# Optimization experiments

Hardware: AMD Instinct MI355X
Metric: run time of the kernel (lower is better)

The kernel has to match this reference:

```python
import jax, jax.numpy as jnp
import numpy as np

B, V = 128, 128000

def setup_inputs() -> dict:
    key = jax.random.key(0)
    k1, k2, k3, k4 = jax.random.split(key, 4)
    logits = jax.random.normal(k1, (B, V), dtype=jnp.float32) * 4.0
    k = jax.random.randint(k2, (B,), 1, 64).astype(jnp.int32)
    p = jax.random.uniform(k3, (B,), dtype=jnp.float32, minval=0.5, maxval=1.0)
    # torch's q.exponential_(): Exp(1) noise = -log(U)
    u = jax.random.uniform(k4, (B, V), dtype=jnp.float32, minval=1e-10, maxval=1.0)
    exp_noise = -jnp.log(u)
    return {"logits": logits, "k": k, "p": p, "exp_noise": exp_noise}

def _apply_top_k_top_p(logits, k, p):
    # ascending sort, matching torch logits.sort(descending=False)
    idx = jnp.argsort(logits, axis=-1)                       # [B, V]
    logits_sort = jnp.take_along_axis(logits, idx, axis=-1)  # [B, V]
    # top-k: threshold is the (V-k)-th smallest value; everything below -> -inf
    thr_pos = (logits.shape[-1] - k.astype(jnp.int32))[:, None]       # [B, 1]
    thr = jnp.take_along_axis(logits_sort, thr_pos, axis=-1)          # [B, 1]
    logits_sort = jnp.where(logits_sort < thr, -jnp.inf, logits_sort)
    # top-p: drop the low-probability tail whose cumulative mass <= 1 - p
    probs_sort = jax.nn.softmax(logits_sort, axis=-1)
    probs_sum = jnp.cumsum(probs_sort, axis=-1)
    top_p_mask = probs_sum <= (1.0 - p)[:, None]
    top_p_mask = top_p_mask.at[:, -1].set(False)  # always keep the max token
    logits_sort = jnp.where(top_p_mask, -jnp.inf, logits_sort)
    # scatter filtered values back to original token positions
    inv = jnp.argsort(idx, axis=-1)
    return jnp.take_along_axis(logits_sort, inv, axis=-1)

def reference(logits, k, p, exp_noise):
    filtered = _apply_top_k_top_p(logits, k, p)
    probs = jax.nn.softmax(filtered.astype(jnp.float32), axis=-1)
    # random_sample: argmax(probs / Exp(1)) == Gumbel-trick categorical sample
    return jnp.argmax(probs / exp_noise, axis=-1)
```

## Files before the change

kernel.cpp:

```cpp
#include <hip/hip_runtime.h>
#include <stdint.h>

#define B_ROWS 128
#define V_COLS 128000
#define BPR 16
#define SLICE (V_COLS / BPR)
#define N4 (SLICE / 4)
#define NTHR 256
#define CAP 2048

__device__ __forceinline__ uint32_t f2u_bits(uint32_t x) {
    return (x & 0x80000000u) ? ~x : (x | 0x80000000u);
}
__device__ __forceinline__ float u2f(uint32_t u) {
    uint32_t x = (u & 0x80000000u) ? (u & 0x7FFFFFFFu) : ~u;
    return __uint_as_float(x);
}

__device__ __forceinline__ bool pair_gt(uint32_t au, uint32_t ai, uint32_t bu, uint32_t bi) {
    return (au > bu) || (au == bu && ai > bi);
}

__device__ __forceinline__ void merge64(uint32_t& au, uint32_t& ai,
                                        uint32_t bu, uint32_t bi, int lane) {
    uint32_t ou = (uint32_t)__shfl_xor((int)bu, 63, 64);
    uint32_t oi = (uint32_t)__shfl_xor((int)bi, 63, 64);
    if (!pair_gt(au, ai, ou, oi)) { au = ou; ai = oi; }
    #pragma unroll
    for (int j = 32; j >= 1; j >>= 1) {
        uint32_t cu = (uint32_t)__shfl_xor((int)au, j, 64);
        uint32_t ci = (uint32_t)__shfl_xor((int)ai, j, 64);
        bool sg = pair_gt(au, ai, cu, ci);
        bool keep = ((lane & j) == 0) ? sg : !sg;
        if (!keep) { au = cu; ai = ci; }
    }
}

__device__ __forceinline__ void wave_sort64(uint32_t& u, uint32_t& i, int lane) {
    #pragma unroll
    for (int ksz = 2; ksz <= 64; ksz <<= 1) {
        #pragma unroll
        for (int j = ksz >> 1; j > 0; j >>= 1) {
            uint32_t ou = (uint32_t)__shfl_xor((int)u, j, 64);
            uint32_t oi = (uint32_t)__shfl_xor((int)i, j, 64);
            bool asc   = (lane & ksz) == 0;
            bool lower = (lane & j) == 0;
            bool sg = pair_gt(u, i, ou, oi);
            bool keep = (asc == lower) ? sg : !sg;
            if (!keep) { u = ou; i = oi; }
        }
    }
}

__device__ __forceinline__ void lds_bitonic_desc(uint32_t* su, uint32_t* si, int NP) {
    const int tid = threadIdx.x;
    for (int ksz = 2; ksz <= NP; ksz <<= 1) {
        for (int j = ksz >> 1; j > 0; j >>= 1) {
            __syncthreads();
            for (int i = tid; i < NP; i += NTHR) {
                int ixj = i ^ j;
                if (ixj > i) {
                    uint32_t ua = su[i], ub = su[ixj];
                    uint32_t ia = si[i], ib = si[ixj];
                    bool a_lt = (ua < ub) || (ua == ub && ia < ib);
                    if (((i & ksz) == 0) ? a_lt : !a_lt) {
                        su[i] = ub; su[ixj] = ua;
                        si[i] = ib; si[ixj] = ia;
                    }
                }
            }
        }
    }
    __syncthreads();
}

__global__ __launch_bounds__(NTHR) void topk_slice_kernel(
    const float* __restrict__ logits, uint2* __restrict__ out_run)
{
    __shared__ uint32_t s_u[CAP];
    __shared__ uint32_t s_i[CAP];
    __shared__ uint32_t s_T[4];
    __shared__ int s_cnt;

    const int blk = blockIdx.x;
    const int row = blk >> 4;
    const int q   = blk & 15;
    const int tid = threadIdx.x;
    const int lane = tid & 63;
    const int wv   = tid >> 6;

    if (tid == 0) s_cnt = 0;

    const uint4* src = (const uint4*)(logits + (size_t)row * V_COLS + (size_t)q * SLICE);

    uint4 g[8];
    #pragma unroll
    for (int j = 0; j < 8; ++j) {
        int i4 = j * NTHR + tid;
        i4 = (i4 < N4) ? i4 : (N4 - 1);
        g[j] = src[i4];
    }
    #pragma unroll
    for (int j = 0; j < 8; ++j) {
        g[j].x = f2u_bits(g[j].x); g[j].y = f2u_bits(g[j].y);
        g[j].z = f2u_bits(g[j].z); g[j].w = f2u_bits(g[j].w);
    }
    if (7 * NTHR + tid >= N4) { g[7].x = 0u; g[7].y = 0u; g[7].z = 0u; g[7].w = 0u; }

    uint32_t mx = 0u;
    #pragma unroll
    for (int j = 0; j < 8; ++j) {
        uint32_t a = g[j].x > g[j].y ? g[j].x : g[j].y;
        uint32_t b = g[j].z > g[j].w ? g[j].z : g[j].w;
        a = a > b ? a : b;
        mx = mx > a ? mx : a;
    }

    uint32_t v = mx;
    #pragma unroll
    for (int ksz = 2; ksz <= 64; ksz <<= 1) {
        #pragma unroll
        for (int j = ksz >> 1; j > 0; j >>= 1) {
            uint32_t o = (uint32_t)__shfl_xor((int)v, j, 64);
            bool asc   = (lane & ksz) == 0;
            bool lower = (lane & j) == 0;
            uint32_t mn = (v < o) ? v : o;
            uint32_t mh = (v < o) ? o : v;
            v = (asc == lower) ? mn : mh;
        }
    }
    uint32_t Tw = (uint32_t)__shfl((int)v, 48, 64);
    if (lane == 0) s_T[wv] = Tw;
    __syncthreads();
    uint32_t T0 = s_T[0] < s_T[1] ? s_T[0] : s_T[1];
    uint32_t T1 = s_T[2] < s_T[3] ? s_T[2] : s_T[3];
    uint32_t T = T0 < T1 ? T0 : T1;

    #pragma unroll
    for (int j = 0; j < 8; ++j) {
        const int base = q * SLICE + (j * NTHR + tid) * 4;
        uint32_t uu0 = g[j].x, uu1 = g[j].y, uu2 = g[j].z, uu3 = g[j].w;
        if (uu0 >= T && uu0 != 0u) { int p = atomicAdd(&s_cnt, 1); if (p < CAP) { s_u[p] = uu0; s_i[p] = (uint32_t)(base + 0); } }
        if (uu1 >= T && uu1 != 0u) { int p = atomicAdd(&s_cnt, 1); if (p < CAP) { s_u[p] = uu1; s_i[p] = (uint32_t)(base + 1); } }
        if (uu2 >= T && uu2 != 0u) { int p = atomicAdd(&s_cnt, 1); if (p < CAP) { s_u[p] = uu2; s_i[p] = (uint32_t)(base + 2); } }
        if (uu3 >= T && uu3 != 0u) { int p = atomicAdd(&s_cnt, 1); if (p < CAP) { s_u[p] = uu3; s_i[p] = (uint32_t)(base + 3); } }
    }
    __syncthreads();
    int cnt = s_cnt; if (cnt > CAP) cnt = CAP;

    if (cnt <= 256) {
        for (int i = cnt + tid; i < 256; i += NTHR) { s_u[i] = 0u; s_i[i] = 0xFFFFFFFFu; }
        __syncthreads();
        uint32_t cu = s_u[wv * 64 + lane];
        uint32_t ci = s_i[wv * 64 + lane];
        wave_sort64(cu, ci, lane);
        s_u[wv * 64 + lane] = cu;
        s_i[wv * 64 + lane] = ci;
        __syncthreads();
        if (wv == 0) {
            uint32_t b1u = s_u[64 + lane];  uint32_t b1i = s_i[64 + lane];
            uint32_t b2u = s_u[128 + lane]; uint32_t b2i = s_i[128 + lane];
            uint32_t b3u = s_u[192 + lane]; uint32_t b3i = s_i[192 + lane];
            merge64(cu, ci, b1u, b1i, lane);
            merge64(b2u, b2i, b3u, b3i, lane);
            merge64(cu, ci, b2u, b2i, lane);
            out_run[blk * 64 + lane] = make_uint2(cu, ci);
        }
    } else {
        int NP = 256; while (NP < cnt) NP <<= 1;
        for (int i = cnt + tid; i < NP; i += NTHR) { s_u[i] = 0u; s_i[i] = 0xFFFFFFFFu; }
        lds_bitonic_desc(s_u, s_i, NP);
        if (tid < 64) out_run[blk * 64 + tid] = make_uint2(s_u[tid], s_i[tid]);
    }
}

__global__ __launch_bounds__(NTHR) void sample_kernel(
    const uint2* __restrict__ runs,
    const int* __restrict__ kk, const float* __restrict__ pp,
    const float* __restrict__ noise, int* __restrict__ out)
{
    __shared__ uint32_t m_u[4 * 64];
    __shared__ uint32_t m_i[4 * 64];
    const int row = blockIdx.x;
    const int tid = threadIdx.x;
    const int lane = tid & 63;
    const int wv   = tid >> 6;

    const uint2* br = runs + (size_t)row * (BPR * 64);

    uint2 r0 = br[(wv * 4 + 0) * 64 + lane];
    uint2 r1 = br[(wv * 4 + 1) * 64 + lane];
    uint2 r2 = br[(wv * 4 + 2) * 64 + lane];
    uint2 r3 = br[(wv * 4 + 3) * 64 + lane];
    uint32_t a0u = r0.x, a0i = r0.y;
    uint32_t a1u = r1.x, a1i = r1.y;
    uint32_t a2u = r2.x, a2i = r2.y;
    uint32_t a3u = r3.x, a3i = r3.y;
    merge64(a0u, a0i, a1u, a1i, lane);
    merge64(a2u, a2i, a3u, a3i, lane);
    merge64(a0u, a0i, a2u, a2i, lane);
    m_u[wv * 64 + lane] = a0u;
    m_i[wv * 64 + lane] = a0i;
    __syncthreads();

    if (wv == 0) {
        uint32_t b1u = m_u[64 + lane];  uint32_t b1i = m_i[64 + lane];
        uint32_t b2u = m_u[128 + lane]; uint32_t b2i = m_i[128 + lane];
        uint32_t b3u = m_u[192 + lane]; uint32_t b3i = m_i[192 + lane];
        merge64(a0u, a0i, b1u, b1i, lane);
        merge64(b2u, b2i, b3u, b3i, lane);
        merge64(a0u, a0i, b2u, b2i, lane);

        float v2 = u2f(a0u);
        uint32_t tok = a0i;
        int k = kk[row];
        if (k > 64) k = 64;
        float p = pp[row];

        float thrv = __shfl(v2, k - 1, 64);
        bool kept = v2 >= thrv;
        float m = __shfl(v2, 0, 64);
        float e = kept ? expf(v2 - m) : 0.0f;

        float denom = e;
        #pragma unroll
        for (int off = 1; off < 64; off <<= 1) denom += __shfl_xor(denom, off, 64);
        float prob = e / denom;

        float cums = prob;
        #pragma unroll
        for (int off = 1; off < 64; off <<= 1) {
            float o = __shfl_down(cums, off, 64);
            cums += (lane + off < 64) ? o : 0.0f;
        }
        bool masked = (cums <= 1.0f - p) && (lane != 0);
        bool surv = kept && !masked;

        float e2 = surv ? e : 0.0f;
        float denom2 = e2;
        #pragma unroll
        for (int off = 1; off < 64; off <<= 1) denom2 += __shfl_xor(denom2, off, 64);

        float score = -1.0f;
        uint32_t bidx = 0xFFFFFFFFu;
        if (surv) {
            float nz = noise[(size_t)row * V_COLS + tok];
            score = (e / denom2) / nz;
            bidx = tok;
        }
        #pragma unroll
        for (int off = 1; off < 64; off <<= 1) {
            float os = __shfl_xor(score, off, 64);
            uint32_t oi = __shfl_xor(bidx, off, 64);
            if (os > score || (os == score && oi < bidx)) { score = os; bidx = oi; }
        }
        if (lane == 0) out[row] = (int)bidx;
    }
}

extern "C" void kernel_launch(void* const* d_in, const int* in_sizes, int n_in,
                              void* d_out, int out_size, void* d_ws, size_t ws_size,
                              hipStream_t stream) {
    const float* logits = (const float*)d_in[0];
    const int* kk       = (const int*)d_in[1];
    const float* pp     = (const float*)d_in[2];
    const float* noise  = (const float*)d_in[3];
    int* out            = (int*)d_out;

    uint2* ws_run = (uint2*)d_ws;

    topk_slice_kernel<<<B_ROWS * BPR, NTHR, 0, stream>>>(logits, ws_run);
    sample_kernel<<<B_ROWS, NTHR, 0, stream>>>(ws_run, kk, pp, noise, out);
}
```

Measured before the change: 27.95 us.

## Halve blocks per row and compute exact block-wide top-64 threshold

Splits each row across 8 blocks instead of 16, so every thread loads 16 uint4 vectors instead of 8. The candidate threshold is now the exact 64th-largest of all per-thread maxima in the block, found with a bitonic merge of the four sorted wave lists, rather than the minimum of four per-wave 16th-largest values. This is meant to shrink the candidate set and the sort work, and it halves the runs the sample kernel has to merge. The cost is fewer blocks (1024 instead of 2048), higher register pressure from the 16 loaded vectors, and two extra barriers.

```diff
diff --git a/kernel.cpp b/kernel.cpp
--- a/kernel.cpp
+++ b/kernel.cpp
@@ -3,10 +3,11 @@
 
 #define B_ROWS 128
 #define V_COLS 128000
-#define BPR 16
+#define BPR 8
 #define SLICE (V_COLS / BPR)
 #define N4 (SLICE / 4)
 #define NTHR 256
+#define LPT 16
 #define CAP 2048
 
 __device__ __forceinline__ uint32_t f2u_bits(uint32_t x) {
@@ -33,6 +34,18 @@
         bool sg = pair_gt(au, ai, cu, ci);
         bool keep = ((lane & j) == 0) ? sg : !sg;
         if (!keep) { au = cu; ai = ci; }
+    }
+}
+
+__device__ __forceinline__ void merge64v(uint32_t& au, uint32_t bu, int lane) {
+    uint32_t ou = (uint32_t)__shfl_xor((int)bu, 63, 64);
+    au = au > ou ? au : ou;
+    #pragma unroll
+    for (int j = 32; j >= 1; j >>= 1) {
+        uint32_t cu = (uint32_t)__shfl_xor((int)au, j, 64);
+        uint32_t mx = au > cu ? au : cu;
+        uint32_t mn = au > cu ? cu : au;
+        au = ((lane & j) == 0) ? mx : mn;
     }
 }
 
@@ -79,12 +92,12 @@
 {
     __shared__ uint32_t s_u[CAP];
     __shared__ uint32_t s_i[CAP];
-    __shared__ uint32_t s_T[4];
+    __shared__ uint32_t s_Tval;
     __shared__ int s_cnt;
 
     const int blk = blockIdx.x;
-    const int row = blk >> 4;
-    const int q   = blk & 15;
+    const int row = blk >> 3;
+    const int q   = blk & 7;
     const int tid = threadIdx.x;
     const int lane = tid & 63;
     const int wv   = tid >> 6;
@@ -93,23 +106,25 @@
 
     const uint4* src = (const uint4*)(logits + (size_t)row * V_COLS + (size_t)q * SLICE);
 
-    uint4 g[8];
-    #pragma unroll
-    for (int j = 0; j < 8; ++j) {
+    uint4 g[LPT];
+    #pragma unroll
+    for (int j = 0; j < LPT; ++j) {
         int i4 = j * NTHR + tid;
         i4 = (i4 < N4) ? i4 : (N4 - 1);
         g[j] = src[i4];
     }
     #pragma unroll
-    for (int j = 0; j < 8; ++j) {
+    for (int j = 0; j < LPT; ++j) {
         g[j].x = f2u_bits(g[j].x); g[j].y = f2u_bits(g[j].y);
         g[j].z = f2u_bits(g[j].z); g[j].w = f2u_bits(g[j].w);
     }
-    if (7 * NTHR + tid >= N4) { g[7].x = 0u; g[7].y = 0u; g[7].z = 0u; g[7].w = 0u; }
+    if ((LPT - 1) * NTHR + tid >= N4) {
+        g[LPT - 1].x = 0u; g[LPT - 1].y = 0u; g[LPT - 1].z = 0u; g[LPT - 1].w = 0u;
+    }
 
     uint32_t mx = 0u;
     #pragma unroll
-    for (int j = 0; j < 8; ++j) {
+    for (int j = 0; j < LPT; ++j) {
         uint32_t a = g[j].x > g[j].y ? g[j].x : g[j].y;
         uint32_t b = g[j].z > g[j].w ? g[j].z : g[j].w;
         a = a > b ? a : b;
@@ -129,15 +144,23 @@
             v = (asc == lower) ? mn : mh;
         }
     }
-    uint32_t Tw = (uint32_t)__shfl((int)v, 48, 64);
-    if (lane == 0) s_T[wv] = Tw;
-    __syncthreads();
-    uint32_t T0 = s_T[0] < s_T[1] ? s_T[0] : s_T[1];
-    uint32_t T1 = s_T[2] < s_T[3] ? s_T[2] : s_T[3];
-    uint32_t T = T0 < T1 ? T0 : T1;
-
-    #pragma unroll
-    for (int j = 0; j < 8; ++j) {
+    s_u[wv * 64 + (63 - lane)] = v;
+    __syncthreads();
+
+    if (wv == 0) {
+        uint32_t t0 = s_u[lane];
+        merge64v(t0, s_u[64 + lane], lane);
+        uint32_t t2 = s_u[128 + lane];
+        merge64v(t2, s_u[192 + lane], lane);
+        merge64v(t0, t2, lane);
+        if (lane == 63) s_Tval = t0;
+    }
+    __syncthreads();
+    const uint32_t T = s_Tval;
+    __syncthreads();
+
+    #pragma unroll
+    for (int j = 0; j < LPT; ++j) {
         const int base = q * SLICE + (j * NTHR + tid) * 4;
         uint32_t uu0 = g[j].x, uu1 = g[j].y, uu2 = g[j].z, uu3 = g[j].w;
         if (uu0 >= T && uu0 != 0u) { int p = atomicAdd(&s_cnt, 1); if (p < CAP) { s_u[p] = uu0; s_i[p] = (uint32_t)(base + 0); } }
@@ -188,17 +211,11 @@
 
     const uint2* br = runs + (size_t)row * (BPR * 64);
 
-    uint2 r0 = br[(wv * 4 + 0) * 64 + lane];
-    uint2 r1 = br[(wv * 4 + 1) * 64 + lane];
-    uint2 r2 = br[(wv * 4 + 2) * 64 + lane];
-    uint2 r3 = br[(wv * 4 + 3) * 64 + lane];
+    uint2 r0 = br[(wv * 2 + 0) * 64 + lane];
+    uint2 r1 = br[(wv * 2 + 1) * 64 + lane];
     uint32_t a0u = r0.x, a0i = r0.y;
     uint32_t a1u = r1.x, a1i = r1.y;
-    uint32_t a2u = r2.x, a2i = r2.y;
-    uint32_t a3u = r3.x, a3i = r3.y;
     merge64(a0u, a0i, a1u, a1i, lane);
-    merge64(a2u, a2i, a3u, a3i, lane);
-    merge64(a0u, a0i, a2u, a2i, lane);
     m_u[wv * 64 + lane] = a0u;
     m_i[wv * 64 + lane] = a0i;
     __syncthreads();
```

Measured after the change: 28.00 us. No clear change (+0.2%).
